# Kernel tuning notes

Measured on AMD Instinct MI355X. Metric: run time of the kernel, lower is better.

The kernel has to match this reference:

```python
import jax, jax.numpy as jnp
import numpy as np

B, N, FOV = 64, 128, 9
CH = [3, 32, 64, 128]
FLAT = CH[-1] * FOV * FOV  # 10368
ENC = 128
K = 3
G1, G2 = 128, 128
A = 5
EPS = 1e-5


def setup_inputs() -> dict:
    key = jax.random.key(0)
    ks = jax.random.split(key, 24)
    d = {}
    d["states"] = jax.random.normal(ks[0], (B, N, 3, FOV, FOV), jnp.float32)
    d["gso"] = jax.random.uniform(ks[1], (B, N, N), jnp.float32)
    i = 2
    for l in range(3):
        cin, cout = CH[l], CH[l + 1]
        d[f"c{l+1}_w"] = jax.random.normal(ks[i], (cout, cin, 3, 3), jnp.float32) * 0.05; i += 1
        d[f"c{l+1}_b"] = jnp.zeros((cout,), jnp.float32)
        d[f"c{l+1}_g"] = jnp.ones((cout,), jnp.float32)
        d[f"c{l+1}_be"] = jnp.zeros((cout,), jnp.float32)
    d["enc_w"] = jax.random.normal(ks[i], (ENC, FLAT), jnp.float32) * (1.0 / np.sqrt(FLAT)); i += 1
    d["enc_b"] = jnp.zeros((ENC,), jnp.float32)
    d["g1_w"] = jax.random.normal(ks[i], (K, G1, ENC), jnp.float32) * (1.0 / np.sqrt(ENC * K)); i += 1
    d["g1_b"] = jnp.zeros((G1,), jnp.float32)
    d["g2_w"] = jax.random.normal(ks[i], (K, G2, G1), jnp.float32) * (1.0 / np.sqrt(G1 * K)); i += 1
    d["g2_b"] = jnp.zeros((G2,), jnp.float32)
    d["act_w"] = jax.random.normal(ks[i], (A, G2), jnp.float32) * (1.0 / np.sqrt(G2)); i += 1
    d["act_b"] = jnp.zeros((A,), jnp.float32)
    return d


def _conv_bn_relu(x, w, b, gamma, beta):
    # 3x3, stride 1, padding 1 -> SAME; NCHW/OIHW
    y = jax.lax.conv_general_dilated(
        x, w, window_strides=(1, 1), padding="SAME",
        dimension_numbers=("NCHW", "OIHW", "NCHW"))
    y = y + b[None, :, None, None]
    # BatchNorm2d in training mode: batch statistics over (N, H, W)
    mu = jnp.mean(y, axis=(0, 2, 3), keepdims=True)
    var = jnp.var(y, axis=(0, 2, 3), keepdims=True)
    y = (y - mu) * jax.lax.rsqrt(var + EPS)
    y = y * gamma[None, :, None, None] + beta[None, :, None, None]
    return jax.nn.relu(y)


def _graph_filter(x, S, w, b):
    # x: [B, F, N], S: [B, N, N], w: [K, G, F] -> y = sum_k W_k (x S^k) + b
    out = jnp.einsum("bfn,gf->bgn", x, w[0])
    xk = x
    for k in range(1, w.shape[0]):
        xk = jnp.einsum("bfn,bnm->bfm", xk, S)
        out = out + jnp.einsum("bfn,gf->bgn", xk, w[k])
    return out + b[None, :, None]


def reference(states, gso,
              c1_w, c1_b, c1_g, c1_be,
              c2_w, c2_b, c2_g, c2_be,
              c3_w, c3_b, c3_g, c3_be,
              enc_w, enc_b, g1_w, g1_b, g2_w, g2_b, act_w, act_b):
    x = states.reshape(B * N, 3, FOV, FOV)
    x = _conv_bn_relu(x, c1_w, c1_b, c1_g, c1_be)
    x = _conv_bn_relu(x, c2_w, c2_b, c2_g, c2_be)
    x = _conv_bn_relu(x, c3_w, c3_b, c3_g, c3_be)
    x = x.reshape(B * N, FLAT)
    x = x @ enc_w.T + enc_b                    # [B*N, ENC]
    x = x.reshape(B, N, ENC).transpose(0, 2, 1)  # [B, F, N]
    x = jax.nn.relu(_graph_filter(x, gso, g1_w, g1_b))
    x = jax.nn.relu(_graph_filter(x, gso, g2_w, g2_b))
    x = x.transpose(0, 2, 1).reshape(B * N, G2)
    logits = x @ act_w.T + act_b
    return logits.reshape(B, N, A)
```

## Files before the change

### kernel.cpp

```cpp
#include <hip/hip_runtime.h>
#include <hip/hip_bf16.h>
#include <stdint.h>


#define NIMG 8192
#define NPIX 81
#define FLAT 10368

typedef __hip_bfloat16 bf16;
typedef short bf16x8 __attribute__((ext_vector_type(8)));
typedef float f32x4 __attribute__((ext_vector_type(4)));

__device__ __forceinline__ float bflo(unsigned u) { return __uint_as_float(u << 16); }
__device__ __forceinline__ float bfhi(unsigned u) { return __uint_as_float(u & 0xffff0000u); }
__device__ __forceinline__ unsigned short f2bf(float f) {
    unsigned u = __float_as_uint(f);
    return (unsigned short)((u + 0x7fff + ((u >> 16) & 1)) >> 16);
}

__device__ __forceinline__ bf16x8 bn8(bf16x8 a, const float* sc, const float* sh) {
    union U { bf16x8 v; unsigned u[4]; } in, out;
    in.v = a;
#pragma unroll
    for (int d = 0; d < 4; d++) {
        float lo = fmaxf(fmaf(bflo(in.u[d]), sc[2 * d],     sh[2 * d]),     0.f);
        float hi = fmaxf(fmaf(bfhi(in.u[d]), sc[2 * d + 1], sh[2 * d + 1]), 0.f);
        out.u[d] = (unsigned)f2bf(lo) | ((unsigned)f2bf(hi) << 16);
    }
    return out.v;
}

__global__ void fill_sentinel(float* __restrict__ out, int n) {
    int i = blockIdx.x * 256 + threadIdx.x;
    if (i < n) out[i] = 1.0e9f;
}

__global__ void prep_w(const float* __restrict__ c1w, const float* __restrict__ c2w,
                       const float* __restrict__ c3w,
                       float* __restrict__ w1t, bf16* __restrict__ w2m,
                       bf16* __restrict__ w3m) {
    int i0 = blockIdx.x * blockDim.x + threadIdx.x;
    int stride = gridDim.x * blockDim.x;
    for (int i = i0; i < 27 * 32; i += stride) w1t[i] = c1w[(i & 31) * 27 + (i >> 5)];
    for (int i = i0; i < 64 * 288; i += stride) {
        int oc = i / 288, r = i - oc * 288, t = r >> 5, ci = r & 31;
        w2m[i] = __float2bfloat16(c2w[oc * 288 + ci * 9 + t]);
    }
    for (int i = i0; i < 128 * 576; i += stride) {
        int oc = i / 576, r = i - oc * 576, t = r >> 6, ci = r & 63;
        w3m[i] = __float2bfloat16(c3w[oc * 576 + ci * 9 + t]);
    }
}

__global__ void prep_enc(const float* __restrict__ encw, bf16* __restrict__ ewb) {
    int i0 = blockIdx.x * blockDim.x + threadIdx.x;
    int stride = gridDim.x * blockDim.x;
    for (int i = i0; i < 128 * FLAT; i += stride) {
        int e = i / FLAT, r = i - e * FLAT;
        int px = r >> 7, ci = r & 127;
        ewb[i] = __float2bfloat16(encw[(size_t)e * FLAT + ci * 81 + px]);
    }
}

__device__ __forceinline__ void load_row(const float* __restrict__ p, float* r) {
    float4 a = *(const float4*)p;
    float4 b = *(const float4*)(p + 4);
    float4 c = *(const float4*)(p + 8);
    r[0]=a.x; r[1]=a.y; r[2]=a.z;  r[3]=a.w;
    r[4]=b.x; r[5]=b.y; r[6]=b.z;  r[7]=b.w;
    r[8]=c.x; r[9]=c.y; r[10]=c.z; r[11]=c.w;
}

__device__ __forceinline__ void conv_body(const float* __restrict__ inp,
                                          const float* __restrict__ wv, float* acc) {
    float rb[3][12];
    load_row(inp, rb[0]);
    load_row(inp + 12, rb[1]);
#pragma unroll
    for (int oy = 0; oy < 9; oy++) {
        load_row(inp + (oy + 2) * 12, rb[(oy + 2) % 3]);
#pragma unroll
        for (int ky = 0; ky < 3; ky++) {
            const float* r = rb[(oy + ky) % 3];
#pragma unroll
            for (int ox = 0; ox < 9; ox++) {
                float s = acc[oy * 9 + ox];
                s = fmaf(r[ox + 0], wv[ky * 3 + 0], s);
                s = fmaf(r[ox + 1], wv[ky * 3 + 1], s);
                s = fmaf(r[ox + 2], wv[ky * 3 + 2], s);
                acc[oy * 9 + ox] = s;
            }
        }
    }
}

__global__ __launch_bounds__(128) void conv1_kernel(const float* __restrict__ xin,
        const float* __restrict__ wt, const float* __restrict__ bias,
        bf16* __restrict__ xout, float* __restrict__ sacc) {
    __shared__ __align__(16) float lds[4 * 3 * 132];
    __shared__ float Sl[128], Ql[128];
    int t = threadIdx.x;
    int img0 = blockIdx.x * 4;
    for (int i = t; i < 4 * 3 * 132; i += 128) lds[i] = 0.f;
    __syncthreads();
    const float* src = xin + (size_t)img0 * 243;
    for (int i = t; i < 4 * 243; i += 128) {
        int il = i / 243, rem = i - il * 243;
        int ci = rem / 81, px = rem - ci * 81;
        lds[(il * 3 + ci) * 132 + (px / 9 + 1) * 12 + (px % 9) + 1] = src[i];
    }
    __syncthreads();
    int oc = t & 31, il = t >> 5;
    const float* base = lds + il * 3 * 132;
    float acc[81];
    float bb = bias[oc];
#pragma unroll
    for (int i = 0; i < 81; i++) acc[i] = bb;
#pragma unroll
    for (int ci = 0; ci < 3; ci++) {
        float wv[9];
#pragma unroll
        for (int k = 0; k < 9; k++) wv[k] = wt[(ci * 9 + k) * 32 + oc];
        conv_body(base + ci * 132, wv, acc);
    }
    bf16* dst = xout + (size_t)(img0 + il) * 81 * 32 + oc;
    float s = 0.f, q = 0.f;
#pragma unroll
    for (int p = 0; p < 81; p++) {
        float v = acc[p];
        s += v; q = fmaf(v, v, q);
        dst[p * 32] = __float2bfloat16(v);
    }
    Sl[il * 32 + oc] = s;
    Ql[il * 32 + oc] = q;
    __syncthreads();
    if (t < 32)
        atomicAdd(&sacc[t], Sl[t] + Sl[32 + t] + Sl[64 + t] + Sl[96 + t]);
    else if (t < 64) {
        int c = t - 32;
        atomicAdd(&sacc[32 + c], Ql[c] + Ql[32 + c] + Ql[64 + c] + Ql[96 + c]);
    }
}

template <int CI, int COT, int OCS>
__global__ __launch_bounds__(256, 2) void conv_tile(const bf16* __restrict__ xin,
        const bf16* __restrict__ wm, const float* __restrict__ bias,
        const float* __restrict__ st, bf16* __restrict__ xout,
        float* __restrict__ sacc) {
    constexpr int NCH = CI / 32;
    constexpr int ROW = 9 * CI;
    constexpr int STEPS = 9 * NCH;
    constexpr int PHASES = STEPS / 9;
    constexpr int HS = STEPS / PHASES;
    __shared__ bf16 Bs[HS * 4 * 64 * 8];
    __shared__ float Ss[2][4][64];

    const int lin = blockIdx.x;
    const int xcd = lin & 7;
    const int slot = lin >> 3;
    constexpr int PSL = 81 * OCS;
    const int igl = slot / PSL;
    const int rem = slot - igl * PSL;
    const int p = rem / OCS;
    const int ob = rem - p * OCS;
    const int ig = xcd * 4 + igl;
    const int oc0 = ob * 64;
    const int py = p / 9, pxx = p - py * 9;
    const int tid = threadIdx.x;
    const int lane = tid & 63, wv = tid >> 6;
    const int m = lane & 15, quad = lane >> 4;
    const long img0 = (long)ig * 256 + wv * 64;

    int qt[9]; bool vt[9];
#pragma unroll
    for (int t = 0; t < 9; t++) {
        int iy = py + t / 3 - 1, ix = pxx + (t % 3) - 1;
        vt[t] = ((unsigned)iy < 9u) && ((unsigned)ix < 9u);
        qt[t] = vt[t] ? iy * 9 + ix : p;
    }

    float scv[NCH][8], shv[NCH][8];
#pragma unroll
    for (int ch = 0; ch < NCH; ch++)
#pragma unroll
        for (int j = 0; j < 8; j++) {
            int ci = ch * 32 + quad * 8 + j;
            scv[ch][j] = st[ci];
            shv[ch][j] = st[CI + ci];
        }

    f32x4 acc[4][4];
#pragma unroll
    for (int nf = 0; nf < 4; nf++) {
        float bb = bias[oc0 + nf * 16 + m];
#pragma unroll
        for (int ms = 0; ms < 4; ms++) {
            acc[ms][nf][0] = bb; acc[ms][nf][1] = bb;
            acc[ms][nf][2] = bb; acc[ms][nf][3] = bb;
        }
    }
    const bf16* ab[4];
#pragma unroll
    for (int ms = 0; ms < 4; ms++)
        ab[ms] = xin + (img0 + ms * 16 + m) * (81 * CI) + quad * 8;

    const bf16* bsl = &Bs[lane * 8];
    const bf16x8 zf = {0, 0, 0, 0, 0, 0, 0, 0};

#pragma unroll
    for (int ph = 0; ph < PHASES; ph++) {
        __syncthreads();
        for (int i = tid; i < HS * 4 * 64; i += 256) {
            int l2 = i & 63, nf = (i >> 6) & 3, sl = i >> 8;
            int s = ph * HS + sl;
            int t = s / NCH, ch = s - t * NCH;
            int mm = l2 & 15, qq = l2 >> 4;
            *(bf16x8*)(&Bs[(size_t)i * 8]) =
                *(const bf16x8*)(wm + (size_t)(oc0 + nf * 16 + mm) * ROW + t * CI + ch * 32 + qq * 8);
        }
        __syncthreads();
#pragma unroll
        for (int sl = 0; sl < HS; sl++) {
            const int s = ph * HS + sl;
            const int t = s / NCH, ch = s - t * NCH;
            bf16x8 bfr[4];
#pragma unroll
            for (int nf = 0; nf < 4; nf++)
                bfr[nf] = *(const bf16x8*)(bsl + (sl * 4 + nf) * 512);
            bf16x8 a[4];
#pragma unroll
            for (int ms = 0; ms < 4; ms++)
                a[ms] = *(const bf16x8*)(ab[ms] + qt[t] * CI + ch * 32);
#pragma unroll
            for (int ms = 0; ms < 4; ms++) {
                bf16x8 v = vt[t] ? bn8(a[ms], scv[ch], shv[ch]) : zf;
#pragma unroll
                for (int nf = 0; nf < 4; nf++)
                    acc[ms][nf] = __builtin_amdgcn_mfma_f32_16x16x32_bf16(v, bfr[nf], acc[ms][nf], 0, 0, 0);
            }
        }
    }

    bf16* orow = xout + (img0 + quad * 4) * (81 * COT) + (size_t)p * COT + oc0 + m;
#pragma unroll
    for (int ms = 0; ms < 4; ms++)
#pragma unroll
        for (int nf = 0; nf < 4; nf++)
#pragma unroll
            for (int r = 0; r < 4; r++)
                orow[(size_t)(ms * 16 + r) * (81 * COT) + nf * 16] =
                    __float2bfloat16(acc[ms][nf][r]);

    float ssum[4], sq[4];
#pragma unroll
    for (int nf = 0; nf < 4; nf++) {
        float s = 0.f, q = 0.f;
#pragma unroll
        for (int ms = 0; ms < 4; ms++)
#pragma unroll
            for (int r = 0; r < 4; r++) {
                float v = acc[ms][nf][r];
                s += v; q = fmaf(v, v, q);
            }
        s += __shfl_xor(s, 16); s += __shfl_xor(s, 32);
        q += __shfl_xor(q, 16); q += __shfl_xor(q, 32);
        ssum[nf] = s; sq[nf] = q;
    }
    if (lane < 16) {
#pragma unroll
        for (int nf = 0; nf < 4; nf++) {
            Ss[0][wv][nf * 16 + lane] = ssum[nf];
            Ss[1][wv][nf * 16 + lane] = sq[nf];
        }
    }
    __syncthreads();
    if (tid < 64) {
        float a = Ss[0][0][tid] + Ss[0][1][tid] + Ss[0][2][tid] + Ss[0][3][tid];
        atomicAdd(&sacc[oc0 + tid], a);
    } else if (tid < 128) {
        int c = tid - 64;
        float a = Ss[1][0][c] + Ss[1][1][c] + Ss[1][2][c] + Ss[1][3][c];
        atomicAdd(&sacc[COT + oc0 + c], a);
    }
}

__global__ __launch_bounds__(256) void enc_mfma(const bf16* __restrict__ x3,
        const bf16* __restrict__ ewb, const float* __restrict__ st,
        float* __restrict__ part) {
    const int lin = blockIdx.x;
    const int xcd = lin & 7;
    const int slot = lin >> 3;
    const int igl = slot >> 3;
    const int combo = slot & 7;
    const int ks = combo >> 1, nh = combo & 1;
    const int ig = xcd * 8 + igl;
    const int lane = threadIdx.x & 63, wv = threadIdx.x >> 6;
    const int m = lane & 15, quad = lane >> 4;
    const long img0 = (long)ig * 128 + wv * 32;

    float scv[4][8], shv[4][8];
#pragma unroll
    for (int cc = 0; cc < 4; cc++)
#pragma unroll
        for (int j = 0; j < 8; j++) {
            int ci = cc * 32 + quad * 8 + j;
            scv[cc][j] = st[ci];
            shv[cc][j] = st[128 + ci];
        }

    f32x4 acc[2][4];
#pragma unroll
    for (int ms = 0; ms < 2; ms++)
#pragma unroll
        for (int nf = 0; nf < 4; nf++) {
            acc[ms][nf][0]=0.f; acc[ms][nf][1]=0.f; acc[ms][nf][2]=0.f; acc[ms][nf][3]=0.f;
        }
    const bf16* ab[2];
    const bf16* bb[4];
#pragma unroll
    for (int ms = 0; ms < 2; ms++)
        ab[ms] = x3 + (img0 + ms * 16 + m) * FLAT + ks * 2592 + quad * 8;
#pragma unroll
    for (int nf = 0; nf < 4; nf++)
        bb[nf] = ewb + (size_t)(nh * 64 + nf * 16 + m) * FLAT + ks * 2592 + quad * 8;

#pragma unroll 3
    for (int c = 0; c < 81; c++) {
        const int cc = (ks + c) & 3;
        bf16x8 Ac[2], Bc[4];
#pragma unroll
        for (int ms = 0; ms < 2; ms++) {
            bf16x8 raw = *(const bf16x8*)(ab[ms] + c * 32);
            Ac[ms] = bn8(raw, scv[cc], shv[cc]);
        }
#pragma unroll
        for (int nf = 0; nf < 4; nf++) Bc[nf] = *(const bf16x8*)(bb[nf] + c * 32);
#pragma unroll
        for (int nf = 0; nf < 4; nf++)
#pragma unroll
            for (int ms = 0; ms < 2; ms++)
                acc[ms][nf] = __builtin_amdgcn_mfma_f32_16x16x32_bf16(Ac[ms], Bc[nf], acc[ms][nf], 0, 0, 0);
    }

    float* pp = part + (size_t)ks * (NIMG * 128) + (img0 + quad * 4) * 128 + nh * 64 + m;
#pragma unroll
    for (int ms = 0; ms < 2; ms++)
#pragma unroll
        for (int nf = 0; nf < 4; nf++)
#pragma unroll
            for (int r = 0; r < 4; r++)
                pp[(ms * 16 + r) * 128 + nf * 16] = acc[ms][nf][r];
}

template <int CO>
__global__ void stats_fin(const float* __restrict__ acc, const float* __restrict__ gamma,
                          const float* __restrict__ beta, float* __restrict__ st) {
    int c = threadIdx.x;
    if (c < CO) {
        const float inv = 1.0f / (8192.0f * 81.0f);
        float m = acc[c] * inv;
        float var = acc[CO + c] * inv - m * m;
        float istd = rsqrtf(var + 1e-5f);
        float sc = istd * gamma[c];
        st[c] = sc;
        st[CO + c] = beta[c] - m * sc;
    }
}

__global__ void enc_reduce(const float* __restrict__ part, const float* __restrict__ encb,
                           float* __restrict__ xT) {
    int i = blockIdx.x * 256 + threadIdx.x;
    const int NP = NIMG * 128;
    if (i < NP) {
        float v = part[i] + part[NP + i] + part[2 * NP + i] + part[3 * NP + i] + encb[i & 127];
        int img = i >> 7, f = i & 127;
        xT[(size_t)(img >> 7) * 16384 + f * 128 + (img & 127)] = v;
    }
}

__global__ __launch_bounds__(256) void mm_xs(const float* __restrict__ A,
        const float* __restrict__ S, float* __restrict__ Y) {
    __shared__ __align__(16) float Sc[32 * 132];
    __shared__ float Acm[32 * 33];
    int b = blockIdx.y, f0 = blockIdx.x * 32;
    int t = threadIdx.x;
    int fl = t & 31, mg = t >> 5;
    const float* Ab = A + (size_t)b * 16384;
    const float* Sb = S + (size_t)b * 16384;
    float acc[16];
#pragma unroll
    for (int j = 0; j < 16; j++) acc[j] = 0.f;
    for (int nc = 0; nc < 128; nc += 32) {
#pragma unroll
        for (int r = 0; r < 4; r++) {
            int i4 = r * 256 + t;
            int nn = i4 >> 5, m4 = (i4 & 31) * 4;
            *(float4*)&Sc[nn * 132 + m4] = *(const float4*)&Sb[(size_t)(nc + nn) * 128 + m4];
        }
#pragma unroll
        for (int r = 0; r < 4; r++) {
            int i = r * 256 + t;
            int ff = i >> 5, nn = i & 31;
            Acm[ff * 33 + nn] = Ab[(size_t)(f0 + ff) * 128 + nc + nn];
        }
        __syncthreads();
#pragma unroll 4
        for (int nn = 0; nn < 32; nn++) {
            float a = Acm[fl * 33 + nn];
#pragma unroll
            for (int j = 0; j < 4; j++) {
                float4 s4 = *(const float4*)&Sc[nn * 132 + mg * 16 + j * 4];
                acc[j*4+0] = fmaf(a, s4.x, acc[j*4+0]);
                acc[j*4+1] = fmaf(a, s4.y, acc[j*4+1]);
                acc[j*4+2] = fmaf(a, s4.z, acc[j*4+2]);
                acc[j*4+3] = fmaf(a, s4.w, acc[j*4+3]);
            }
        }
        __syncthreads();
    }
    float* yb = Y + (size_t)b * 16384 + (size_t)(f0 + fl) * 128 + mg * 16;
#pragma unroll
    for (int j = 0; j < 4; j++)
        *(float4*)&yb[j * 4] = make_float4(acc[j*4], acc[j*4+1], acc[j*4+2], acc[j*4+3]);
}

__global__ __launch_bounds__(256) void gf_combine(const float* __restrict__ Z0,
        const float* __restrict__ Z1, const float* __restrict__ Z2,
        const float* __restrict__ W, const float* __restrict__ bias,
        float* __restrict__ out) {
    __shared__ __align__(16) float Zc[32 * 132];
    __shared__ float Wc[32 * 33];
    int b = blockIdx.y, g0 = blockIdx.x * 32;
    int t = threadIdx.x;
    int gl = t & 31, mg = t >> 5;
    float acc[16];
    float bb = bias[g0 + gl];
#pragma unroll
    for (int j = 0; j < 16; j++) acc[j] = bb;
    const float* Zs[3] = {Z0 + (size_t)b * 16384, Z1 + (size_t)b * 16384, Z2 + (size_t)b * 16384};
    for (int j3 = 0; j3 < 3; j3++) {
        const float* Zb = Zs[j3];
        const float* Wj = W + j3 * 16384;
        for (int fc = 0; fc < 128; fc += 32) {
#pragma unroll
            for (int r = 0; r < 4; r++) {
                int i4 = r * 256 + t;
                int ff = i4 >> 5, m4 = (i4 & 31) * 4;
                *(float4*)&Zc[ff * 132 + m4] = *(const float4*)&Zb[(size_t)(fc + ff) * 128 + m4];
            }
#pragma unroll
            for (int r = 0; r < 4; r++) {
                int i = r * 256 + t;
                int gg = i >> 5, ff = i & 31;
                Wc[gg * 33 + ff] = Wj[(size_t)(g0 + gg) * 128 + fc + ff];
            }
            __syncthreads();
#pragma unroll 4
            for (int ff = 0; ff < 32; ff++) {
                float w = Wc[gl * 33 + ff];
#pragma unroll
                for (int j = 0; j < 4; j++) {
                    float4 z4 = *(const float4*)&Zc[ff * 132 + mg * 16 + j * 4];
                    acc[j*4+0] = fmaf(w, z4.x, acc[j*4+0]);
                    acc[j*4+1] = fmaf(w, z4.y, acc[j*4+1]);
                    acc[j*4+2] = fmaf(w, z4.z, acc[j*4+2]);
                    acc[j*4+3] = fmaf(w, z4.w, acc[j*4+3]);
                }
            }
            __syncthreads();
        }
    }
    float* ob = out + (size_t)b * 16384 + (size_t)(g0 + gl) * 128 + mg * 16;
#pragma unroll
    for (int j = 0; j < 4; j++)
        *(float4*)&ob[j * 4] = make_float4(fmaxf(acc[j*4], 0.f), fmaxf(acc[j*4+1], 0.f),
                                           fmaxf(acc[j*4+2], 0.f), fmaxf(acc[j*4+3], 0.f));
}

__global__ __launch_bounds__(128) void act_kernel(const float* __restrict__ X,
        const float* __restrict__ aw, const float* __restrict__ ab,
        float* __restrict__ out) {
    int b = blockIdx.x, n = threadIdx.x;
    float acc[5];
#pragma unroll
    for (int a = 0; a < 5; a++) acc[a] = ab[a];
    const float* xb = X + (size_t)b * 16384 + n;
#pragma unroll 4
    for (int g = 0; g < 128; g++) {
        float v = xb[(size_t)g * 128];
#pragma unroll
        for (int a = 0; a < 5; a++) acc[a] = fmaf(v, aw[a * 128 + g], acc[a]);
    }
    float* ob = out + ((size_t)b * 128 + n) * 5;
#pragma unroll
    for (int a = 0; a < 5; a++) ob[a] = acc[a];
}

extern "C" void kernel_launch(void* const* d_in, const int* in_sizes, int n_in,
                              void* d_out, int out_size, void* d_ws, size_t ws_size,
                              hipStream_t stream) {
    const float* states = (const float*)d_in[0];
    const float* gso    = (const float*)d_in[1];
    const float* c1w  = (const float*)d_in[2];
    const float* c1b  = (const float*)d_in[3];
    const float* c1g  = (const float*)d_in[4];
    const float* c1be = (const float*)d_in[5];
    const float* c2w  = (const float*)d_in[6];
    const float* c2b  = (const float*)d_in[7];
    const float* c2g  = (const float*)d_in[8];
    const float* c2be = (const float*)d_in[9];
    const float* c3w  = (const float*)d_in[10];
    const float* c3b  = (const float*)d_in[11];
    const float* c3g  = (const float*)d_in[12];
    const float* c3be = (const float*)d_in[13];
    const float* encw = (const float*)d_in[14];
    const float* encb = (const float*)d_in[15];
    const float* g1w  = (const float*)d_in[16];
    const float* g1b  = (const float*)d_in[17];
    const float* g2w  = (const float*)d_in[18];
    const float* g2b  = (const float*)d_in[19];
    const float* aw   = (const float*)d_in[20];
    const float* ab   = (const float*)d_in[21];
    float* out = (float*)d_out;
    char* ws = (char*)d_ws;

    size_t o = 0;
    auto take = [&](size_t bytes) { size_t r = o; o += (bytes + 255) & ~(size_t)255; return r; };
    const size_t o_x3  = take((size_t)NIMG * 81 * 128 * 2);
    const size_t o_x2  = take((size_t)NIMG * 81 * 64 * 2);
    const size_t o_w1t = take(27 * 32 * 4);
    const size_t o_w2m = take(64 * 288 * 2);
    const size_t o_w3m = take(128 * 576 * 2);
    const size_t o_acc = take(448 * 4);
    const size_t o_st1 = take(2 * 32 * 4);
    const size_t o_st2 = take(2 * 64 * 4);
    const size_t o_st3 = take(2 * 128 * 4);
    if (ws_size < o) {
        fill_sentinel<<<(out_size + 255) / 256, 256, 0, stream>>>(out, out_size);
        return;
    }

    const size_t o_x1 = o_x3;
    const size_t o_ewb  = o_x2;
    const size_t o_part = o_x2 + 2654208;
    const size_t o_xT   = o_part + 16777216;
    const size_t o_y1   = o_xT + 4194304;
    const size_t o_y2   = o_y1 + 4194304;
    const size_t o_G1   = o_y2 + 4194304;
    const size_t o_G2   = o_G1 + 4194304;

    bf16* x1 = (bf16*)(ws + o_x1);
    bf16* x2 = (bf16*)(ws + o_x2);
    bf16* x3 = (bf16*)(ws + o_x3);
    float* w1t = (float*)(ws + o_w1t);
    bf16* w2m = (bf16*)(ws + o_w2m);
    bf16* w3m = (bf16*)(ws + o_w3m);
    float* acc1 = (float*)(ws + o_acc);
    float* acc2 = acc1 + 64;
    float* acc3 = acc1 + 192;
    float* st1 = (float*)(ws + o_st1);
    float* st2 = (float*)(ws + o_st2);
    float* st3 = (float*)(ws + o_st3);
    bf16* ewb = (bf16*)(ws + o_ewb);
    float* partp = (float*)(ws + o_part);
    float* xT = (float*)(ws + o_xT);
    float* y1 = (float*)(ws + o_y1);
    float* y2 = (float*)(ws + o_y2);
    float* xG1 = (float*)(ws + o_G1);
    float* xG2 = (float*)(ws + o_G2);

    hipMemsetAsync(ws + o_acc, 0, 448 * 4, stream);
    prep_w<<<128, 256, 0, stream>>>(c1w, c2w, c3w, w1t, w2m, w3m);

    conv1_kernel<<<2048, 128, 0, stream>>>(states, w1t, c1b, x1, acc1);
    stats_fin<32><<<1, 32, 0, stream>>>(acc1, c1g, c1be, st1);

    conv_tile<32, 64, 1><<<2592, 256, 0, stream>>>(x1, w2m, c2b, st1, x2, acc2);
    stats_fin<64><<<1, 64, 0, stream>>>(acc2, c2g, c2be, st2);

    conv_tile<64, 128, 2><<<5184, 256, 0, stream>>>(x2, w3m, c3b, st2, x3, acc3);
    stats_fin<128><<<1, 128, 0, stream>>>(acc3, c3g, c3be, st3);

    prep_enc<<<2048, 256, 0, stream>>>(encw, ewb);
    enc_mfma<<<512, 256, 0, stream>>>(x3, ewb, st3, partp);
    enc_reduce<<<4096, 256, 0, stream>>>(partp, encb, xT);

    mm_xs<<<dim3(4, 64), 256, 0, stream>>>(xT, gso, y1);
    mm_xs<<<dim3(4, 64), 256, 0, stream>>>(y1, gso, y2);
    gf_combine<<<dim3(4, 64), 256, 0, stream>>>(xT, y1, y2, g1w, g1b, xG1);

    mm_xs<<<dim3(4, 64), 256, 0, stream>>>(xG1, gso, y1);
    mm_xs<<<dim3(4, 64), 256, 0, stream>>>(y1, gso, y2);
    gf_combine<<<dim3(4, 64), 256, 0, stream>>>(xG1, y1, y2, g2w, g2b, xG2);

    act_kernel<<<64, 128, 0, stream>>>(xG2, aw, ab, out);
}
```

Measured before the change: 796.9 us.

## Store activations pixel-chunk-major with images contiguous for coalesced MFMA loads

Changes intermediate activation layout from per-image [px][ch] to [px][ch/32][img][32] across conv1 output, conv2/conv3 input and output, and the encoder GEMM, and reorders the bf16 encoder weights to match. Adjacent MFMA rows (consecutive images) now read contiguous memory, improving coalescing and cache line use versus widely strided per-image rows. Writes in conv1 become strided per pixel, and index math grows.

```diff
diff --git a/kernel.cpp b/kernel.cpp
--- a/kernel.cpp
+++ b/kernel.cpp
@@ -57,8 +57,9 @@
     int stride = gridDim.x * blockDim.x;
     for (int i = i0; i < 128 * FLAT; i += stride) {
         int e = i / FLAT, r = i - e * FLAT;
-        int px = r >> 7, ci = r & 127;
-        ewb[i] = __float2bfloat16(encw[(size_t)e * FLAT + ci * 81 + px]);
+        int kk = r >> 5, c32 = r & 31;
+        int px = kk >> 2, cc = kk & 3;
+        ewb[i] = __float2bfloat16(encw[(size_t)e * FLAT + (cc * 32 + c32) * 81 + px]);
     }
 }
 
@@ -123,13 +124,14 @@
         for (int k = 0; k < 9; k++) wv[k] = wt[(ci * 9 + k) * 32 + oc];
         conv_body(base + ci * 132, wv, acc);
     }
-    bf16* dst = xout + (size_t)(img0 + il) * 81 * 32 + oc;
+    bf16* dst = xout + (size_t)(img0 + il) * 32 + oc;
+    const size_t PXS = (size_t)NIMG * 32;
     float s = 0.f, q = 0.f;
 #pragma unroll
     for (int p = 0; p < 81; p++) {
         float v = acc[p];
         s += v; q = fmaf(v, v, q);
-        dst[p * 32] = __float2bfloat16(v);
+        dst[p * PXS] = __float2bfloat16(v);
     }
     Sl[il * 32 + oc] = s;
     Ql[il * 32 + oc] = q;
@@ -148,10 +150,12 @@
         const float* __restrict__ st, bf16* __restrict__ xout,
         float* __restrict__ sacc) {
     constexpr int NCH = CI / 32;
+    constexpr int NCHO = COT / 32;
     constexpr int ROW = 9 * CI;
     constexpr int STEPS = 9 * NCH;
     constexpr int PHASES = STEPS / 9;
     constexpr int HS = STEPS / PHASES;
+    constexpr size_t CSTRIDE = (size_t)NIMG * 32;
     __shared__ bf16 Bs[HS * 4 * 64 * 8];
     __shared__ float Ss[2][4][64];
 
@@ -202,7 +206,7 @@
     const bf16* ab[4];
 #pragma unroll
     for (int ms = 0; ms < 4; ms++)
-        ab[ms] = xin + (img0 + ms * 16 + m) * (81 * CI) + quad * 8;
+        ab[ms] = xin + (img0 + ms * 16 + m) * 32 + quad * 8;
 
     const bf16* bsl = &Bs[lane * 8];
     const bf16x8 zf = {0, 0, 0, 0, 0, 0, 0, 0};
@@ -230,7 +234,7 @@
             bf16x8 a[4];
 #pragma unroll
             for (int ms = 0; ms < 4; ms++)
-                a[ms] = *(const bf16x8*)(ab[ms] + qt[t] * CI + ch * 32);
+                a[ms] = *(const bf16x8*)(ab[ms] + (size_t)(qt[t] * NCH + ch) * CSTRIDE);
 #pragma unroll
             for (int ms = 0; ms < 4; ms++) {
                 bf16x8 v = vt[t] ? bn8(a[ms], scv[ch], shv[ch]) : zf;
@@ -241,15 +245,18 @@
         }
     }
 
-    bf16* orow = xout + (img0 + quad * 4) * (81 * COT) + (size_t)p * COT + oc0 + m;
+    const int och = oc0 >> 5;
 #pragma unroll
     for (int ms = 0; ms < 4; ms++)
 #pragma unroll
-        for (int nf = 0; nf < 4; nf++)
+        for (int nf = 0; nf < 4; nf++) {
+            bf16* orow = xout
+                + (((size_t)p * NCHO + och + (nf >> 1)) * NIMG + img0 + ms * 16 + quad * 4) * 32
+                + (nf & 1) * 16 + m;
 #pragma unroll
             for (int r = 0; r < 4; r++)
-                orow[(size_t)(ms * 16 + r) * (81 * COT) + nf * 16] =
-                    __float2bfloat16(acc[ms][nf][r]);
+                orow[r * 32] = __float2bfloat16(acc[ms][nf][r]);
+        }
 
     float ssum[4], sq[4];
 #pragma unroll
@@ -297,6 +304,7 @@
     const int lane = threadIdx.x & 63, wv = threadIdx.x >> 6;
     const int m = lane & 15, quad = lane >> 4;
     const long img0 = (long)ig * 128 + wv * 32;
+    constexpr size_t CSTRIDE = (size_t)NIMG * 32;
 
     float scv[4][8], shv[4][8];
 #pragma unroll
@@ -319,10 +327,10 @@
     const bf16* bb[4];
 #pragma unroll
     for (int ms = 0; ms < 2; ms++)
-        ab[ms] = x3 + (img0 + ms * 16 + m) * FLAT + ks * 2592 + quad * 8;
+        ab[ms] = x3 + (size_t)(ks * 81) * CSTRIDE + (img0 + ms * 16 + m) * 32 + quad * 8;
 #pragma unroll
     for (int nf = 0; nf < 4; nf++)
-        bb[nf] = ewb + (size_t)(nh * 64 + nf * 16 + m) * FLAT + ks * 2592 + quad * 8;
+        bb[nf] = ewb + (size_t)(nh * 64 + nf * 16 + m) * FLAT + ks * 81 * 32 + quad * 8;
 
 #pragma unroll 3
     for (int c = 0; c < 81; c++) {
@@ -330,7 +338,7 @@
         bf16x8 Ac[2], Bc[4];
 #pragma unroll
         for (int ms = 0; ms < 2; ms++) {
-            bf16x8 raw = *(const bf16x8*)(ab[ms] + c * 32);
+            bf16x8 raw = *(const bf16x8*)(ab[ms] + (size_t)c * CSTRIDE);
             Ac[ms] = bn8(raw, scv[cc], shv[cc]);
         }
 #pragma unroll
@@ -526,8 +534,8 @@
 
     size_t o = 0;
     auto take = [&](size_t bytes) { size_t r = o; o += (bytes + 255) & ~(size_t)255; return r; };
-    const size_t o_x3  = take((size_t)NIMG * 81 * 128 * 2);
-    const size_t o_x2  = take((size_t)NIMG * 81 * 64 * 2);
+    const size_t o_x3  = take((size_t)81 * 4 * NIMG * 32 * 2);
+    const size_t o_x2  = take((size_t)81 * 2 * NIMG * 32 * 2);
     const size_t o_w1t = take(27 * 32 * 4);
     const size_t o_w2m = take(64 * 288 * 2);
     const size_t o_w3m = take(128 * 576 * 2);
```

New measurement: 752.9 us. 5.5% less time.
